# Kernel optimization log

Measured on AMD Instinct MI355X. Metric: run time of the kernel, lower is better.

Reference implementation:

```python
import jax, jax.numpy as jnp
import numpy as np

BATCH = 2048
IN_DIM = 4096
OUT_DIM = 1024
N_EDGES = 16384  # mat_wann.connection_count
CONSTANT_WEIGHT = 1.0


def setup_inputs() -> dict:
    key = jax.random.key(0)
    k1, k2, k3 = jax.random.split(key, 3)
    x = jax.random.normal(k1, (BATCH, IN_DIM), dtype=jnp.float32)
    # one scalar Linear(1,1,bias=False) per connection, all init to constant_weight
    weights = jnp.ones((N_EDGES,), dtype=jnp.float32) * CONSTANT_WEIGHT
    # edge list: src input column, dst output node (sorted => segment-friendly)
    edge_src = jax.random.randint(k2, (N_EDGES,), 0, IN_DIM, dtype=jnp.int32)
    edge_dst = jnp.sort(jax.random.randint(k3, (N_EDGES,), 0, OUT_DIM, dtype=jnp.int32))
    return {"x": x, "weights": weights, "edge_src": edge_src, "edge_dst": edge_dst}


def reference(x, weights, edge_src, edge_dst):
    # gather per-edge input column and apply the per-edge scalar linear
    contrib = x[:, edge_src] * weights[None, :]              # [B, E]
    # scatter-add (segment-reduce) per-edge contributions into output nodes
    node_sums = jax.ops.segment_sum(contrib.T, edge_dst, num_segments=OUT_DIM)  # [OUT_DIM, B]
    # per-node activation (self.activations[...]); nodes with no incoming edges
    # stay zero, matching torch.zeros for empty rows since tanh(0)=0
    h = jnp.tanh(node_sums.T)                                 # [B, OUT_DIM]
    # activation_list applied to concatenated outputs
    return jax.nn.sigmoid(h)
```

## Files before the change

### kernel.cpp

```cpp
#include <hip/hip_runtime.h>
#include <hip/hip_fp16.h>
#include <math.h>

#define BATCH   2048
#define IN_DIM  4096
#define OUT_DIM 1024
#define N_EDGES 16384

#define R    4
#define NG   16
#define LCAP 64


__device__ __forceinline__ float hbits_to_f(unsigned int u) {
    __half_raw r; r.x = (unsigned short)u;
    return __half2float(r);
}

__device__ __forceinline__ unsigned int f_to_bf16(float f) {
    unsigned int u = __float_as_uint(f);
    return (u + 0x7FFFu + ((u >> 16) & 1u)) >> 16;
}

__device__ __forceinline__ float act(float a) {
    const float e2 = __expf(2.0f * a);
    const float h = 1.0f - 2.0f / (e2 + 1.0f);
    return 1.0f / (1.0f + __expf(-h));
}

__global__ __launch_bounds__(256) void prep_kernel(
        const int* __restrict__ edge_dst,
        const int* __restrict__ edge_src,
        const float* __restrict__ weights,
        uint4* __restrict__ rec4,
        int* __restrict__ gm4arr) {
    __shared__ int s_lo[64], s_deg[64], s_gm;
    const int g = blockIdx.x, t = threadIdx.x, l = t & 63;
    if (t == 0) s_gm = 8;
    __syncthreads();
    if (t < 64) {
        const int n = g * 64 + l;
        int lo = 0, hi = N_EDGES;
        while (lo < hi) { int m = (lo + hi) >> 1; if (edge_dst[m] < n) lo = m + 1; else hi = m; }
        int lo2 = lo, hi2 = N_EDGES;
        while (lo2 < hi2) { int m = (lo2 + hi2) >> 1; if (edge_dst[m] < n + 1) lo2 = m + 1; else hi2 = m; }
        int deg = lo2 - lo; if (deg > LCAP) deg = LCAP;
        s_lo[l] = lo; s_deg[l] = deg;
        atomicMax(&s_gm, deg);
    }
    __syncthreads();
    const int gm4 = (s_gm + 3) & ~3;
    if (t == 0) gm4arr[g] = gm4;
    const int nch  = gm4 >> 2;
    const int nchw = (nch + 1) & ~1;
    const int lo = s_lo[l], deg = s_deg[l];
    for (int c = t >> 6; c < nchw; c += 4) {
        unsigned int v[4];
#pragma unroll
        for (int k = 0; k < 4; k++) {
            const int i = c * 4 + k;
            unsigned int p = 0;
            if (i < deg) {
                const int e = lo + i;
                const __half hw = __float2half(weights[e]);
                p = ((unsigned int)edge_src[e] << 3) |
                    ((unsigned int)__half_as_ushort(hw) << 16);
            }
            v[k] = p;
        }
        rec4[(size_t)(g * (LCAP / 4) + c) * 64 + l] =
            make_uint4(v[0], v[1], v[2], v[3]);
    }
}

#define SLOT(u)                                                            \
    {                                                                      \
        const uint2 xv = *(const uint2*)((const char*)xs + ((u) & 0xFFF8u));\
        const float wv = hbits_to_f((u) >> 16);                            \
        b0 = fmaf(wv, __uint_as_float(xv.x << 16), b0);                    \
        b1 = fmaf(wv, __uint_as_float(xv.x & 0xFFFF0000u), b1);            \
        b2 = fmaf(wv, __uint_as_float(xv.y << 16), b2);                    \
        b3 = fmaf(wv, __uint_as_float(xv.y & 0xFFFF0000u), b3);            \
    }
#define PROC(q) { SLOT((q).x); SLOT((q).y); SLOT((q).z); SLOT((q).w); }

#define RUN_GROUP(ep, nch, qa_in, qb_in, A0, A1, A2, A3)                   \
    {                                                                      \
        float b0 = 0.0f, b1 = 0.0f, b2 = 0.0f, b3 = 0.0f;                  \
        uint4 qa = qa_in, qb = qb_in;                                      \
        int c = 0;                                                         \
        for (; c + 2 < nch; c += 2) {                                      \
            const uint4 qc = ep[(c + 2) * 64];                             \
            const uint4 qd = ep[(c + 3) * 64];                             \
            PROC(qa); PROC(qb);                                            \
            qa = qc; qb = qd;                                              \
        }                                                                  \
        PROC(qa);                                                          \
        if (c + 1 < nch) PROC(qb);                                         \
        A0 = b0; A1 = b1; A2 = b2; A3 = b3;                                \
    }

__global__ __launch_bounds__(512, 4) void fused_kernel(
        const float* __restrict__ x,
        const uint4* __restrict__ rec4,
        const int* __restrict__ gm4arr,
        float* __restrict__ out) {
    __shared__ uint2 xs[IN_DIM];

    const int brow = blockIdx.x * R;
    const int t = threadIdx.x;
    const int w = t >> 6, l = t & 63;

    const int g0 = 2 * w, g1 = 2 * w + 1;
    const uint4* ep0 = rec4 + (size_t)(g0 * (LCAP / 4)) * 64 + l;
    const uint4* ep1 = rec4 + (size_t)(g1 * (LCAP / 4)) * 64 + l;

    uint4 q0a = ep0[0], q0b = ep0[64];
    uint4 q1a = ep1[0], q1b = ep1[64];
    const int nch0 = __builtin_amdgcn_readfirstlane(gm4arr[g0]) >> 2;
    const int nch1 = __builtin_amdgcn_readfirstlane(gm4arr[g1]) >> 2;

    const float* xr = x + (size_t)brow * IN_DIM;
#pragma unroll
    for (int k = 0; k < IN_DIM / 512; k++) {
        const int c = t + k * 512;
        const unsigned int r0 = f_to_bf16(xr[c]);
        const unsigned int r1 = f_to_bf16(xr[IN_DIM + c]);
        const unsigned int r2 = f_to_bf16(xr[2 * IN_DIM + c]);
        const unsigned int r3 = f_to_bf16(xr[3 * IN_DIM + c]);
        xs[c] = make_uint2((r1 << 16) | r0, (r3 << 16) | r2);
    }
    __syncthreads();

    float a00, a01, a02, a03, a10, a11, a12, a13;
    RUN_GROUP(ep0, nch0, q0a, q0b, a00, a01, a02, a03);
    RUN_GROUP(ep1, nch1, q1a, q1b, a10, a11, a12, a13);

    const int node0 = g0 * 64 + l, node1 = g1 * 64 + l;
    out[(size_t)(brow + 0) * OUT_DIM + node0] = act(a00);
    out[(size_t)(brow + 1) * OUT_DIM + node0] = act(a01);
    out[(size_t)(brow + 2) * OUT_DIM + node0] = act(a02);
    out[(size_t)(brow + 3) * OUT_DIM + node0] = act(a03);
    out[(size_t)(brow + 0) * OUT_DIM + node1] = act(a10);
    out[(size_t)(brow + 1) * OUT_DIM + node1] = act(a11);
    out[(size_t)(brow + 2) * OUT_DIM + node1] = act(a12);
    out[(size_t)(brow + 3) * OUT_DIM + node1] = act(a13);
}

extern "C" void kernel_launch(void* const* d_in, const int* in_sizes, int n_in,
                              void* d_out, int out_size, void* d_ws, size_t ws_size,
                              hipStream_t stream) {
    const float* x        = (const float*)d_in[0];
    const float* weights  = (const float*)d_in[1];
    const int*   edge_src = (const int*)d_in[2];
    const int*   edge_dst = (const int*)d_in[3];
    float*       out      = (float*)d_out;

    uint4* rec4   = (uint4*)d_ws;
    int*   gm4arr = (int*)((char*)d_ws +
                           (size_t)NG * (LCAP / 4) * 64 * sizeof(uint4));

    prep_kernel<<<NG, 256, 0, stream>>>(edge_dst, edge_src, weights,
                                        rec4, gm4arr);

    fused_kernel<<<BATCH / R, 512, 0, stream>>>(x, rec4, gm4arr, out);
}
```

Baseline: 95.88 us.

## Process eight batch rows per block and split node groups across grid y

```diff
diff --git a/kernel.cpp b/kernel.cpp
--- a/kernel.cpp
+++ b/kernel.cpp
@@ -7,7 +7,7 @@
 #define OUT_DIM 1024
 #define N_EDGES 16384
 
-#define R    4
+#define R    8
 #define NG   16
 #define LCAP 64
 
@@ -20,6 +20,15 @@
 __device__ __forceinline__ unsigned int f_to_bf16(float f) {
     unsigned int u = __float_as_uint(f);
     return (u + 0x7FFFu + ((u >> 16) & 1u)) >> 16;
+}
+__device__ __forceinline__ unsigned int pack2(float a, float b) {
+    return (f_to_bf16(b) << 16) | f_to_bf16(a);
+}
+__device__ __forceinline__ float blo(unsigned int u) {
+    return __uint_as_float(u << 16);
+}
+__device__ __forceinline__ float bhi(unsigned int u) {
+    return __uint_as_float(u & 0xFFFF0000u);
 }
 
 __device__ __forceinline__ float act(float a) {
@@ -63,7 +72,7 @@
             if (i < deg) {
                 const int e = lo + i;
                 const __half hw = __float2half(weights[e]);
-                p = ((unsigned int)edge_src[e] << 3) |
+                p = ((unsigned int)edge_src[e] << 4) |
                     ((unsigned int)__half_as_ushort(hw) << 16);
             }
             v[k] = p;
@@ -75,76 +84,74 @@
 
 #define SLOT(u)                                                            \
     {                                                                      \
-        const uint2 xv = *(const uint2*)((const char*)xs + ((u) & 0xFFF8u));\
+        const uint4 xv = *(const uint4*)((const char*)xs + ((u) & 0xFFF0u));\
         const float wv = hbits_to_f((u) >> 16);                            \
-        b0 = fmaf(wv, __uint_as_float(xv.x << 16), b0);                    \
-        b1 = fmaf(wv, __uint_as_float(xv.x & 0xFFFF0000u), b1);            \
-        b2 = fmaf(wv, __uint_as_float(xv.y << 16), b2);                    \
-        b3 = fmaf(wv, __uint_as_float(xv.y & 0xFFFF0000u), b3);            \
+        a0 = fmaf(wv, blo(xv.x), a0); a1 = fmaf(wv, bhi(xv.x), a1);        \
+        a2 = fmaf(wv, blo(xv.y), a2); a3 = fmaf(wv, bhi(xv.y), a3);        \
+        a4 = fmaf(wv, blo(xv.z), a4); a5 = fmaf(wv, bhi(xv.z), a5);        \
+        a6 = fmaf(wv, blo(xv.w), a6); a7 = fmaf(wv, bhi(xv.w), a7);        \
     }
 #define PROC(q) { SLOT((q).x); SLOT((q).y); SLOT((q).z); SLOT((q).w); }
-
-#define RUN_GROUP(ep, nch, qa_in, qb_in, A0, A1, A2, A3)                   \
-    {                                                                      \
-        float b0 = 0.0f, b1 = 0.0f, b2 = 0.0f, b3 = 0.0f;                  \
-        uint4 qa = qa_in, qb = qb_in;                                      \
-        int c = 0;                                                         \
-        for (; c + 2 < nch; c += 2) {                                      \
-            const uint4 qc = ep[(c + 2) * 64];                             \
-            const uint4 qd = ep[(c + 3) * 64];                             \
-            PROC(qa); PROC(qb);                                            \
-            qa = qc; qb = qd;                                              \
-        }                                                                  \
-        PROC(qa);                                                          \
-        if (c + 1 < nch) PROC(qb);                                         \
-        A0 = b0; A1 = b1; A2 = b2; A3 = b3;                                \
-    }
 
 __global__ __launch_bounds__(512, 4) void fused_kernel(
         const float* __restrict__ x,
         const uint4* __restrict__ rec4,
         const int* __restrict__ gm4arr,
         float* __restrict__ out) {
-    __shared__ uint2 xs[IN_DIM];
+    __shared__ uint4 xs[IN_DIM];
 
     const int brow = blockIdx.x * R;
     const int t = threadIdx.x;
     const int w = t >> 6, l = t & 63;
 
-    const int g0 = 2 * w, g1 = 2 * w + 1;
-    const uint4* ep0 = rec4 + (size_t)(g0 * (LCAP / 4)) * 64 + l;
-    const uint4* ep1 = rec4 + (size_t)(g1 * (LCAP / 4)) * 64 + l;
+    const int g = blockIdx.y * 8 + w;
+    const uint4* ep = rec4 + (size_t)(g * (LCAP / 4)) * 64 + l;
 
-    uint4 q0a = ep0[0], q0b = ep0[64];
-    uint4 q1a = ep1[0], q1b = ep1[64];
-    const int nch0 = __builtin_amdgcn_readfirstlane(gm4arr[g0]) >> 2;
-    const int nch1 = __builtin_amdgcn_readfirstlane(gm4arr[g1]) >> 2;
+    uint4 qa = ep[0], qb = ep[64];
+    const int nch = __builtin_amdgcn_readfirstlane(gm4arr[g]) >> 2;
 
     const float* xr = x + (size_t)brow * IN_DIM;
 #pragma unroll
-    for (int k = 0; k < IN_DIM / 512; k++) {
-        const int c = t + k * 512;
-        const unsigned int r0 = f_to_bf16(xr[c]);
-        const unsigned int r1 = f_to_bf16(xr[IN_DIM + c]);
-        const unsigned int r2 = f_to_bf16(xr[2 * IN_DIM + c]);
-        const unsigned int r3 = f_to_bf16(xr[3 * IN_DIM + c]);
-        xs[c] = make_uint2((r1 << 16) | r0, (r3 << 16) | r2);
+    for (int q = 0; q < IN_DIM / (512 * 4); q++) {
+        const int c0 = (t + q * 512) * 4;
+        float4 r[R];
+#pragma unroll
+        for (int i = 0; i < R; i++)
+            r[i] = *(const float4*)(xr + (size_t)i * IN_DIM + c0);
+#pragma unroll
+        for (int k = 0; k < 4; k++) {
+            const float e0 = k == 0 ? r[0].x : k == 1 ? r[0].y : k == 2 ? r[0].z : r[0].w;
+            const float e1 = k == 0 ? r[1].x : k == 1 ? r[1].y : k == 2 ? r[1].z : r[1].w;
+            const float e2 = k == 0 ? r[2].x : k == 1 ? r[2].y : k == 2 ? r[2].z : r[2].w;
+            const float e3 = k == 0 ? r[3].x : k == 1 ? r[3].y : k == 2 ? r[3].z : r[3].w;
+            const float e4 = k == 0 ? r[4].x : k == 1 ? r[4].y : k == 2 ? r[4].z : r[4].w;
+            const float e5 = k == 0 ? r[5].x : k == 1 ? r[5].y : k == 2 ? r[5].z : r[5].w;
+            const float e6 = k == 0 ? r[6].x : k == 1 ? r[6].y : k == 2 ? r[6].z : r[6].w;
+            const float e7 = k == 0 ? r[7].x : k == 1 ? r[7].y : k == 2 ? r[7].z : r[7].w;
+            xs[c0 + k] = make_uint4(pack2(e0, e1), pack2(e2, e3),
+                                    pack2(e4, e5), pack2(e6, e7));
+        }
     }
     __syncthreads();
 
-    float a00, a01, a02, a03, a10, a11, a12, a13;
-    RUN_GROUP(ep0, nch0, q0a, q0b, a00, a01, a02, a03);
-    RUN_GROUP(ep1, nch1, q1a, q1b, a10, a11, a12, a13);
+    float a0 = 0.f, a1 = 0.f, a2 = 0.f, a3 = 0.f;
+    float a4 = 0.f, a5 = 0.f, a6 = 0.f, a7 = 0.f;
+    int c = 0;
+    for (; c + 2 < nch; c += 2) {
+        const uint4 qc = ep[(c + 2) * 64];
+        const uint4 qd = ep[(c + 3) * 64];
+        PROC(qa); PROC(qb);
+        qa = qc; qb = qd;
+    }
+    PROC(qa);
+    if (c + 1 < nch) PROC(qb);
 
-    const int node0 = g0 * 64 + l, node1 = g1 * 64 + l;
-    out[(size_t)(brow + 0) * OUT_DIM + node0] = act(a00);
-    out[(size_t)(brow + 1) * OUT_DIM + node0] = act(a01);
-    out[(size_t)(brow + 2) * OUT_DIM + node0] = act(a02);
-    out[(size_t)(brow + 3) * OUT_DIM + node0] = act(a03);
-    out[(size_t)(brow + 0) * OUT_DIM + node1] = act(a10);
-    out[(size_t)(brow + 1) * OUT_DIM + node1] = act(a11);
-    out[(size_t)(brow + 2) * OUT_DIM + node1] = act(a12);
-    out[(size_t)(brow + 3) * OUT_DIM + node1] = act(a13);
+    const int node = g * 64 + l;
+    float* o = out + (size_t)brow * OUT_DIM + node;
+    o[0 * OUT_DIM] = act(a0); o[1 * OUT_DIM] = act(a1);
+    o[2 * OUT_DIM] = act(a2); o[3 * OUT_DIM] = act(a3);
+    o[4 * OUT_DIM] = act(a4); o[5 * OUT_DIM] = act(a5);
+    o[6 * OUT_DIM] = act(a6); o[7 * OUT_DIM] = act(a7);
 }
 
 extern "C" void kernel_launch(void* const* d_in, const int* in_sizes, int n_in,
@@ -163,5 +170,6 @@
     prep_kernel<<<NG, 256, 0, stream>>>(edge_dst, edge_src, weights,
                                         rec4, gm4arr);
 
-    fused_kernel<<<BATCH / R, 512, 0, stream>>>(x, rec4, gm4arr, out);
+    dim3 grid(BATCH / R, 2);
+    fused_kernel<<<grid, 512, 0, stream>>>(x, rec4, gm4arr, out);
 }
```

Result: no change. 96.02 us (+0.1%).
